# Performance work log

Hardware: AMD Instinct MI355X
Metric: run time of the kernel (lower is better)

The kernel has to match this reference:

```python
import jax, jax.numpy as jnp
from jax import lax
import numpy as np

S = 2        # scale_factor
K = 5        # upsample_kernel_size
M = 64       # m_channels
C_IN = 128

def setup_inputs() -> dict:
    key = jax.random.key(0)
    k1, k2, k3, k4, k5 = jax.random.split(key, 5)
    B, C, H, W = 8, C_IN, 64, 64
    x = jax.random.normal(k1, (B, C, H, W), dtype=jnp.float32)
    compress_w = jax.random.normal(k2, (M, C, 1, 1), dtype=jnp.float32) * 0.05
    compress_b = jax.random.normal(k3, (M,), dtype=jnp.float32) * 0.05
    n_out = K * K * S * S  # 100
    encoder_w = jax.random.normal(k4, (n_out, M, 3, 3), dtype=jnp.float32) * 0.05
    encoder_b = jax.random.normal(k5, (n_out,), dtype=jnp.float32) * 0.05
    return {"x": x, "compress_w": compress_w, "compress_b": compress_b,
            "encoder_w": encoder_w, "encoder_b": encoder_b}

def _carafe(x, compress_w, compress_b, encoder_w, encoder_b):
    B, C, H, W = x.shape
    k, s = K, S
    nH, nW = s * H, s * W
    # 1x1 compress conv
    m = jnp.einsum('bchw,mc->bmhw', x, compress_w[:, :, 0, 0]) + compress_b[None, :, None, None]
    # 3x3 encoder conv, stride 1, pad 1 (SAME)
    ker = lax.conv_general_dilated(m, encoder_w, window_strides=(1, 1), padding='SAME',
                                   dimension_numbers=('NCHW', 'OIHW', 'NCHW'))
    ker = ker + encoder_b[None, :, None, None]  # (B, k*k*s*s, H, W)
    # PixelShuffle(s): (B, k*k, s, s, H, W) -> (B, k*k, H, s, W, s) -> (B, k*k, nH, nW)
    ker = ker.reshape(B, k * k, s, s, H, W).transpose(0, 1, 4, 2, 5, 3).reshape(B, k * k, nH, nW)
    ker = jax.nn.softmax(ker, axis=1)
    # Unfold(k, stride=1, pad=k//2): stack k*k shifted views, ordering (kh outer, kw inner)
    pad = k // 2
    xp = jnp.pad(x, ((0, 0), (0, 0), (pad, pad), (pad, pad)))
    patches = jnp.stack([xp[:, :, i:i + H, j:j + W] for i in range(k) for j in range(k)],
                        axis=2)  # (B, C, k*k, H, W)
    # nearest upsample by s on spatial dims
    up = jnp.repeat(jnp.repeat(patches, s, axis=3), s, axis=4)  # (B, C, k*k, nH, nW)
    # weighted local sum
    out = jnp.sum(up * ker[:, None, :, :, :], axis=2)  # (B, C, nH, nW)
    return out

def reference(x, compress_w, compress_b, encoder_w, encoder_b):
    return _carafe(x, compress_w, compress_b, encoder_w, encoder_b)
```

## Files before the change

### kernel.cpp

```cpp
#include <hip/hip_runtime.h>
#include <math.h>


typedef __attribute__((ext_vector_type(8))) short short8;
typedef __attribute__((ext_vector_type(4))) float floatx4;
typedef __attribute__((ext_vector_type(2))) float v2f;

__device__ __forceinline__ unsigned short f2bf(float f) {
  union { float f; unsigned int u; } v; v.f = f;
  unsigned int u = v.u + 0x7fffu + ((v.u >> 16) & 1u);
  return (unsigned short)(u >> 16);
}
__device__ __forceinline__ void unpack2(unsigned int u, float& lo, float& hi) {
  union { unsigned int u; float f; } a, b;
  a.u = u << 16; b.u = u & 0xffff0000u;
  lo = a.f; hi = b.f;
}
__device__ __forceinline__ v2f unpack2v(unsigned int u) {
  union { unsigned int u; float f; } a, b;
  a.u = u << 16; b.u = u & 0xffff0000u;
  return (v2f){a.f, b.f};
}

__global__ __launch_bounds__(256) void k_prep_pad(
    const float* __restrict__ ew, const float* __restrict__ cw,
    unsigned short* __restrict__ a_prep, float* __restrict__ cwT,
    unsigned short* __restrict__ xpad) {
  const int blk = blockIdx.x;
  if (blk < 2448) {
    int idx = blk * 256 + (int)threadIdx.x;
    *(uint4*)&xpad[(size_t)idx * 8] = make_uint4(0u, 0u, 0u, 0u);
  } else {
    int idx = (blk - 2448) * 256 + (int)threadIdx.x;
    if (idx < 9 * 128 * 64) {
      int mo = idx & 63;
      int n = (idx >> 6) & 127;
      int tap = idx >> 13;
      float v = (n < 100) ? ew[(n * 64 + mo) * 9 + tap] : 0.f;
      a_prep[idx] = f2bf(v);
    } else {
      int r = idx - 9 * 128 * 64;
      int c = r >> 6, mo = r & 63;
      cwT[c * 64 + mo] = cw[mo * 128 + c];
    }
  }
}

__global__ __launch_bounds__(256) void k_compress(
    const float* __restrict__ x, const float* __restrict__ cwT,
    const float* __restrict__ cb, unsigned short* __restrict__ m_t,
    unsigned short* __restrict__ xpad) {
  __shared__ __align__(16) unsigned short ms[64][72];
  const int b = blockIdx.x >> 6;
  const int h = blockIdx.x & 63;
  const int wv = __builtin_amdgcn_readfirstlane((int)(threadIdx.x >> 6));
  const int lane = (int)(threadIdx.x & 63);
  const int mo0 = wv * 16;

  float acc[16];
#pragma unroll
  for (int k = 0; k < 16; ++k) acc[k] = 0.f;

  const float* xp = x + (((size_t)b * 128) * 64 + h) * 64 + lane;
  const float* wp = cwT + mo0;
  unsigned short* xpd =
      xpad + ((size_t)(b * 128) * 4896) + (h + 2) * 72 + 2 + lane;

#pragma unroll 4
  for (int c = 0; c < 128; ++c) {
    float xv = xp[(size_t)c * 4096];
    if ((c >> 5) == wv)
      xpd[(size_t)c * 4896] = f2bf(xv);
#pragma unroll
    for (int k = 0; k < 16; ++k)
      acc[k] = fmaf(xv, wp[c * 64 + k], acc[k]);
  }

#pragma unroll
  for (int k = 0; k < 16; ++k) acc[k] += cb[mo0 + k];

#pragma unroll
  for (int k = 0; k < 8; ++k) {
    unsigned int p = ((unsigned int)f2bf(acc[2 * k + 1]) << 16) | f2bf(acc[2 * k]);
    *(unsigned int*)&ms[lane][mo0 + 2 * k] = p;
  }
  __syncthreads();
  const int t = threadIdx.x;
#pragma unroll
  for (int rep = 0; rep < 2; ++rep) {
    int idx = t + rep * 256;
    uint4 v = *(const uint4*)&ms[idx >> 3][(idx & 7) * 8];
    *(uint4*)&m_t[(size_t)blockIdx.x * 4096 + idx * 8] = v;
  }
}

__global__ __launch_bounds__(512, 4) void k_main(
    const unsigned short* __restrict__ m_t, const unsigned short* __restrict__ a_prep,
    const float* __restrict__ eb, const unsigned short* __restrict__ xpad,
    float* __restrict__ out) {
  __shared__ __align__(16) float raw[128 * 66];
  unsigned short* m_s = (unsigned short*)raw;
  unsigned short* wgt_s = (unsigned short*)raw;
  const int b = blockIdx.x >> 6;
  const int h = blockIdx.x & 63;
  const int t = threadIdx.x;

  for (int idx = t; idx < 3 * 64 * 8; idx += 512) {
    int r = idx >> 9;
    int rem = idx & 511;
    int w = rem >> 3, u = rem & 7;
    int hh = h + r - 1;
    uint4 val = make_uint4(0u, 0u, 0u, 0u);
    if (hh >= 0 && hh < 64)
      val = *(const uint4*)&m_t[(((b * 64 + hh) * 64 + w) * 64) + u * 8];
    *(uint4*)&m_s[(r * 64 + w) * 72 + u * 8] = val;
  }
  __syncthreads();

  const int wave = t >> 6, lane = t & 63;
  const int quad = lane >> 4, col = lane & 15;
  const int nbase = wave * 16;

  const floatx4 z4 = {0.f, 0.f, 0.f, 0.f};
  floatx4 acc[4];
#pragma unroll
  for (int p = 0; p < 4; ++p) acc[p] = z4;

  const short8 z8 = {0, 0, 0, 0, 0, 0, 0, 0};

#pragma unroll
  for (int tap = 0; tap < 9; ++tap) {
    const int dh = tap / 3, dw = tap % 3;
#pragma unroll
    for (int half = 0; half < 2; ++half) {
      const int mo0 = half * 32;
      short8 a0 = *(const short8*)&a_prep[((tap * 128 + nbase + col) * 64) + mo0 + quad * 8];
#pragma unroll
      for (int p = 0; p < 4; ++p) {
        int wsrc = p * 16 + col + dw - 1;
        int wc = min(max(wsrc, 0), 63);
        short8 bf = *(const short8*)&m_s[(dh * 64 + wc) * 72 + mo0 + quad * 8];
        if (wsrc < 0 || wsrc > 63) bf = z8;
        acc[p] = __builtin_amdgcn_mfma_f32_16x16x32_bf16(a0, bf, acc[p], 0, 0, 0);
      }
    }
  }

  __syncthreads();
#pragma unroll
  for (int p = 0; p < 4; ++p)
#pragma unroll
    for (int r = 0; r < 4; ++r)
      raw[(nbase + quad * 4 + r) * 66 + p * 16 + col] = acc[p][r];
  __syncthreads();

  float v[25];
  float inv = 0.f;
  if (t < 256) {
    const int q = wave;
    float mx = -1e30f;
#pragma unroll
    for (int kk = 0; kk < 25; ++kk) {
      v[kk] = raw[(kk * 4 + q) * 66 + lane] + eb[kk * 4 + q];
      mx = fmaxf(mx, v[kk]);
    }
    float s = 0.f;
#pragma unroll
    for (int kk = 0; kk < 25; ++kk) {
      v[kk] = __expf(v[kk] - mx);
      s += v[kk];
    }
    inv = 1.f / s;
  }
  __syncthreads();
  if (t < 256) {
    const int q = wave;
    const int ohl = q >> 1;
    const int owp = 2 * lane + (q & 1);
#pragma unroll
    for (int kk = 0; kk < 25; ++kk)
      wgt_s[(ohl * 25 + kk) * 128 + owp] = f2bf(v[kk] * inv);
  }
  __syncthreads();

  const int wg = t & 15;
  const int cg = t >> 4;
  const int w0 = wg * 4;
  const int c0 = cg * 4;

  const unsigned short* xb =
      xpad + ((size_t)(b * 128 + c0) * 4896) + h * 72 + w0;

  v2f accB[2][4][4];
#pragma unroll
  for (int oh = 0; oh < 2; ++oh)
#pragma unroll
    for (int ch = 0; ch < 4; ++ch)
#pragma unroll
      for (int k = 0; k < 4; ++k) accB[oh][ch][k] = (v2f){0.f, 0.f};

  for (int i = 0; i < 5; ++i) {
    float xr[4][8];
#pragma unroll
    for (int ch = 0; ch < 4; ++ch) {
      uint4 rawv = *(const uint4*)(xb + ch * 4896 + i * 72);
      unpack2(rawv.x, xr[ch][0], xr[ch][1]);
      unpack2(rawv.y, xr[ch][2], xr[ch][3]);
      unpack2(rawv.z, xr[ch][4], xr[ch][5]);
      unpack2(rawv.w, xr[ch][6], xr[ch][7]);
    }
#pragma unroll
    for (int j = 0; j < 5; ++j) {
      const int ij = i * 5 + j;
#pragma unroll
      for (int oh = 0; oh < 2; ++oh) {
        uint4 wr = *(const uint4*)&wgt_s[(oh * 25 + ij) * 128 + w0 * 2];
        v2f wp[4];
        wp[0] = unpack2v(wr.x);
        wp[1] = unpack2v(wr.y);
        wp[2] = unpack2v(wr.z);
        wp[3] = unpack2v(wr.w);
#pragma unroll
        for (int k = 0; k < 4; ++k)
#pragma unroll
          for (int ch = 0; ch < 4; ++ch) {
            float xv = xr[ch][k + j];
            v2f xvv = {xv, xv};
            accB[oh][ch][k] += xvv * wp[k];
          }
      }
    }
  }

#pragma unroll
  for (int ch = 0; ch < 4; ++ch)
#pragma unroll
    for (int oh = 0; oh < 2; ++oh) {
      float* orow =
          out + ((size_t)(b * 128 + c0 + ch) * 128 + (2 * h + oh)) * 128 + w0 * 2;
      float4 f0 = make_float4(accB[oh][ch][0].x, accB[oh][ch][0].y,
                              accB[oh][ch][1].x, accB[oh][ch][1].y);
      float4 f1 = make_float4(accB[oh][ch][2].x, accB[oh][ch][2].y,
                              accB[oh][ch][3].x, accB[oh][ch][3].y);
      *(float4*)orow = f0;
      *(float4*)(orow + 4) = f1;
    }
}

extern "C" void kernel_launch(void* const* d_in, const int* in_sizes, int n_in,
                              void* d_out, int out_size, void* d_ws, size_t ws_size,
                              hipStream_t stream) {
  (void)in_sizes; (void)n_in; (void)out_size; (void)ws_size;
  const float* x  = (const float*)d_in[0];
  const float* cw = (const float*)d_in[1];
  const float* cb = (const float*)d_in[2];
  const float* ew = (const float*)d_in[3];
  const float* eb = (const float*)d_in[4];
  float* out = (float*)d_out;

  char* wsb = (char*)d_ws;
  unsigned short* m_t    = (unsigned short*)(wsb);
  unsigned short* a_prep = (unsigned short*)(wsb + 4194304);
  unsigned short* xpad   = (unsigned short*)(wsb + 4341760);
  float*          cwT    = (float*)(wsb + 14368768);

  k_prep_pad<<<dim3(2768), dim3(256), 0, stream>>>(ew, cw, a_prep, cwT, xpad);
  k_compress<<<dim3(512), dim3(256), 0, stream>>>(x, cwT, cb, m_t, xpad);
  k_main<<<dim3(512), dim3(512), 0, stream>>>(m_t, a_prep, eb, xpad, out);
}
```

Measured before the change: 153.5 us.

## Halve k_main block size with more work per wave and swizzle block-to-row mapping

k_main now runs 256 threads per block instead of 512. Each wave computes two 16-row MFMA output tiles, sharing the B fragment loads, and every thread handles both channel halves in a loop in the weighted-sum phase, so all threads also take part in the softmax. Block indices in both k_compress and k_main are swizzled so that consecutive blocks map to rows spread across the image, which changes L2 and XCD locality for the neighbouring-row reads. This trades thread-level parallelism and occupancy constraints for more per-thread work and register pressure, and the launch bound no longer requests four blocks per CU.

```diff
diff --git a/kernel.cpp b/kernel.cpp
--- a/kernel.cpp
+++ b/kernel.cpp
@@ -20,6 +20,12 @@
   union { unsigned int u; float f; } a, b;
   a.u = u << 16; b.u = u & 0xffff0000u;
   return (v2f){a.f, b.f};
+}
+__device__ __forceinline__ void swizzle_bh(int blk, int& b, int& h) {
+  int x = blk & 7;
+  int i = blk >> 3;
+  b = i >> 3;
+  h = x * 8 + (i & 7);
 }
 
 __global__ __launch_bounds__(256) void k_prep_pad(
@@ -51,8 +57,8 @@
     const float* __restrict__ cb, unsigned short* __restrict__ m_t,
     unsigned short* __restrict__ xpad) {
   __shared__ __align__(16) unsigned short ms[64][72];
-  const int b = blockIdx.x >> 6;
-  const int h = blockIdx.x & 63;
+  int b, h;
+  swizzle_bh(blockIdx.x, b, h);
   const int wv = __builtin_amdgcn_readfirstlane((int)(threadIdx.x >> 6));
   const int lane = (int)(threadIdx.x & 63);
   const int mo0 = wv * 16;
@@ -86,45 +92,48 @@
   }
   __syncthreads();
   const int t = threadIdx.x;
+  const size_t mbase = (size_t)(b * 64 + h) * 4096;
 #pragma unroll
   for (int rep = 0; rep < 2; ++rep) {
     int idx = t + rep * 256;
     uint4 v = *(const uint4*)&ms[idx >> 3][(idx & 7) * 8];
-    *(uint4*)&m_t[(size_t)blockIdx.x * 4096 + idx * 8] = v;
-  }
-}
-
-__global__ __launch_bounds__(512, 4) void k_main(
+    *(uint4*)&m_t[mbase + idx * 8] = v;
+  }
+}
+
+__global__ __launch_bounds__(256) void k_main(
     const unsigned short* __restrict__ m_t, const unsigned short* __restrict__ a_prep,
     const float* __restrict__ eb, const unsigned short* __restrict__ xpad,
     float* __restrict__ out) {
   __shared__ __align__(16) float raw[128 * 66];
   unsigned short* m_s = (unsigned short*)raw;
   unsigned short* wgt_s = (unsigned short*)raw;
-  const int b = blockIdx.x >> 6;
-  const int h = blockIdx.x & 63;
+  int b, h;
+  swizzle_bh(blockIdx.x, b, h);
   const int t = threadIdx.x;
 
-  for (int idx = t; idx < 3 * 64 * 8; idx += 512) {
+  for (int idx = t; idx < 3 * 64 * 8; idx += 256) {
     int r = idx >> 9;
     int rem = idx & 511;
     int w = rem >> 3, u = rem & 7;
     int hh = h + r - 1;
     uint4 val = make_uint4(0u, 0u, 0u, 0u);
     if (hh >= 0 && hh < 64)
-      val = *(const uint4*)&m_t[(((b * 64 + hh) * 64 + w) * 64) + u * 8];
+      val = *(const uint4*)&m_t[(((size_t)(b * 64 + hh) * 64 + w) * 64) + u * 8];
     *(uint4*)&m_s[(r * 64 + w) * 72 + u * 8] = val;
   }
   __syncthreads();
 
   const int wave = t >> 6, lane = t & 63;
   const int quad = lane >> 4, col = lane & 15;
-  const int nbase = wave * 16;
+  const int nbase = wave * 32;
 
   const floatx4 z4 = {0.f, 0.f, 0.f, 0.f};
-  floatx4 acc[4];
-#pragma unroll
-  for (int p = 0; p < 4; ++p) acc[p] = z4;
+  floatx4 acc[2][4];
+#pragma unroll
+  for (int i = 0; i < 2; ++i)
+#pragma unroll
+    for (int p = 0; p < 4; ++p) acc[i][p] = z4;
 
   const short8 z8 = {0, 0, 0, 0, 0, 0, 0, 0};
 
@@ -135,46 +144,47 @@
     for (int half = 0; half < 2; ++half) {
       const int mo0 = half * 32;
       short8 a0 = *(const short8*)&a_prep[((tap * 128 + nbase + col) * 64) + mo0 + quad * 8];
+      short8 a1 = *(const short8*)&a_prep[((tap * 128 + nbase + 16 + col) * 64) + mo0 + quad * 8];
 #pragma unroll
       for (int p = 0; p < 4; ++p) {
         int wsrc = p * 16 + col + dw - 1;
         int wc = min(max(wsrc, 0), 63);
         short8 bf = *(const short8*)&m_s[(dh * 64 + wc) * 72 + mo0 + quad * 8];
         if (wsrc < 0 || wsrc > 63) bf = z8;
-        acc[p] = __builtin_amdgcn_mfma_f32_16x16x32_bf16(a0, bf, acc[p], 0, 0, 0);
+        acc[0][p] = __builtin_amdgcn_mfma_f32_16x16x32_bf16(a0, bf, acc[0][p], 0, 0, 0);
+        acc[1][p] = __builtin_amdgcn_mfma_f32_16x16x32_bf16(a1, bf, acc[1][p], 0, 0, 0);
       }
     }
   }
 
   __syncthreads();
 #pragma unroll
-  for (int p = 0; p < 4; ++p)
-#pragma unroll
-    for (int r = 0; r < 4; ++r)
-      raw[(nbase + quad * 4 + r) * 66 + p * 16 + col] = acc[p][r];
-  __syncthreads();
-
+  for (int i = 0; i < 2; ++i)
+#pragma unroll
+    for (int p = 0; p < 4; ++p)
+#pragma unroll
+      for (int r = 0; r < 4; ++r)
+        raw[(nbase + i * 16 + quad * 4 + r) * 66 + p * 16 + col] = acc[i][p][r];
+  __syncthreads();
+
+  const int q = wave;
   float v[25];
-  float inv = 0.f;
-  if (t < 256) {
-    const int q = wave;
-    float mx = -1e30f;
-#pragma unroll
-    for (int kk = 0; kk < 25; ++kk) {
-      v[kk] = raw[(kk * 4 + q) * 66 + lane] + eb[kk * 4 + q];
-      mx = fmaxf(mx, v[kk]);
-    }
-    float s = 0.f;
-#pragma unroll
-    for (int kk = 0; kk < 25; ++kk) {
-      v[kk] = __expf(v[kk] - mx);
-      s += v[kk];
-    }
-    inv = 1.f / s;
-  }
-  __syncthreads();
-  if (t < 256) {
-    const int q = wave;
+  float mx = -1e30f;
+#pragma unroll
+  for (int kk = 0; kk < 25; ++kk) {
+    v[kk] = raw[(kk * 4 + q) * 66 + lane] + eb[kk * 4 + q];
+    mx = fmaxf(mx, v[kk]);
+  }
+  float s = 0.f;
+#pragma unroll
+  for (int kk = 0; kk < 25; ++kk) {
+    v[kk] = __expf(v[kk] - mx);
+    s += v[kk];
+  }
+  float inv = 1.f / s;
+
+  __syncthreads();
+  {
     const int ohl = q >> 1;
     const int owp = 2 * lane + (q & 1);
 #pragma unroll
@@ -186,65 +196,67 @@
   const int wg = t & 15;
   const int cg = t >> 4;
   const int w0 = wg * 4;
-  const int c0 = cg * 4;
-
-  const unsigned short* xb =
-      xpad + ((size_t)(b * 128 + c0) * 4896) + h * 72 + w0;
-
-  v2f accB[2][4][4];
-#pragma unroll
-  for (int oh = 0; oh < 2; ++oh)
+
+  for (int chalf = 0; chalf < 2; ++chalf) {
+    const int c0 = chalf * 64 + cg * 4;
+    const unsigned short* xb =
+        xpad + ((size_t)(b * 128 + c0) * 4896) + h * 72 + w0;
+
+    v2f accB[2][4][4];
+#pragma unroll
+    for (int oh = 0; oh < 2; ++oh)
+#pragma unroll
+      for (int ch = 0; ch < 4; ++ch)
+#pragma unroll
+        for (int k = 0; k < 4; ++k) accB[oh][ch][k] = (v2f){0.f, 0.f};
+
+    for (int i = 0; i < 5; ++i) {
+      float xr[4][8];
+#pragma unroll
+      for (int ch = 0; ch < 4; ++ch) {
+        uint4 rawv = *(const uint4*)(xb + ch * 4896 + i * 72);
+        unpack2(rawv.x, xr[ch][0], xr[ch][1]);
+        unpack2(rawv.y, xr[ch][2], xr[ch][3]);
+        unpack2(rawv.z, xr[ch][4], xr[ch][5]);
+        unpack2(rawv.w, xr[ch][6], xr[ch][7]);
+      }
+#pragma unroll
+      for (int j = 0; j < 5; ++j) {
+        const int ij = i * 5 + j;
+#pragma unroll
+        for (int oh = 0; oh < 2; ++oh) {
+          uint4 wr = *(const uint4*)&wgt_s[(oh * 25 + ij) * 128 + w0 * 2];
+          v2f wp[4];
+          wp[0] = unpack2v(wr.x);
+          wp[1] = unpack2v(wr.y);
+          wp[2] = unpack2v(wr.z);
+          wp[3] = unpack2v(wr.w);
+#pragma unroll
+          for (int k = 0; k < 4; ++k)
+#pragma unroll
+            for (int ch = 0; ch < 4; ++ch) {
+              float xv = xr[ch][k + j];
+              v2f xvv = {xv, xv};
+              accB[oh][ch][k] += xvv * wp[k];
+            }
+        }
+      }
+    }
+
 #pragma unroll
     for (int ch = 0; ch < 4; ++ch)
 #pragma unroll
-      for (int k = 0; k < 4; ++k) accB[oh][ch][k] = (v2f){0.f, 0.f};
-
-  for (int i = 0; i < 5; ++i) {
-    float xr[4][8];
-#pragma unroll
-    for (int ch = 0; ch < 4; ++ch) {
-      uint4 rawv = *(const uint4*)(xb + ch * 4896 + i * 72);
-      unpack2(rawv.x, xr[ch][0], xr[ch][1]);
-      unpack2(rawv.y, xr[ch][2], xr[ch][3]);
-      unpack2(rawv.z, xr[ch][4], xr[ch][5]);
-      unpack2(rawv.w, xr[ch][6], xr[ch][7]);
-    }
-#pragma unroll
-    for (int j = 0; j < 5; ++j) {
-      const int ij = i * 5 + j;
-#pragma unroll
       for (int oh = 0; oh < 2; ++oh) {
-        uint4 wr = *(const uint4*)&wgt_s[(oh * 25 + ij) * 128 + w0 * 2];
-        v2f wp[4];
-        wp[0] = unpack2v(wr.x);
-        wp[1] = unpack2v(wr.y);
-        wp[2] = unpack2v(wr.z);
-        wp[3] = unpack2v(wr.w);
-#pragma unroll
-        for (int k = 0; k < 4; ++k)
-#pragma unroll
-          for (int ch = 0; ch < 4; ++ch) {
-            float xv = xr[ch][k + j];
-            v2f xvv = {xv, xv};
-            accB[oh][ch][k] += xvv * wp[k];
-          }
-      }
-    }
-  }
-
-#pragma unroll
-  for (int ch = 0; ch < 4; ++ch)
-#pragma unroll
-    for (int oh = 0; oh < 2; ++oh) {
-      float* orow =
-          out + ((size_t)(b * 128 + c0 + ch) * 128 + (2 * h + oh)) * 128 + w0 * 2;
-      float4 f0 = make_float4(accB[oh][ch][0].x, accB[oh][ch][0].y,
-                              accB[oh][ch][1].x, accB[oh][ch][1].y);
-      float4 f1 = make_float4(accB[oh][ch][2].x, accB[oh][ch][2].y,
-                              accB[oh][ch][3].x, accB[oh][ch][3].y);
-      *(float4*)orow = f0;
-      *(float4*)(orow + 4) = f1;
-    }
+        float* orow =
+            out + ((size_t)(b * 128 + c0 + ch) * 128 + (2 * h + oh)) * 128 + w0 * 2;
+        float4 f0 = make_float4(accB[oh][ch][0].x, accB[oh][ch][0].y,
+                                accB[oh][ch][1].x, accB[oh][ch][1].y);
+        float4 f1 = make_float4(accB[oh][ch][2].x, accB[oh][ch][2].y,
+                                accB[oh][ch][3].x, accB[oh][ch][3].y);
+        *(float4*)orow = f0;
+        *(float4*)(orow + 4) = f1;
+      }
+  }
 }
 
 extern "C" void kernel_launch(void* const* d_in, const int* in_sizes, int n_in,
@@ -266,5 +278,5 @@
 
   k_prep_pad<<<dim3(2768), dim3(256), 0, stream>>>(ew, cw, a_prep, cwT, xpad);
   k_compress<<<dim3(512), dim3(256), 0, stream>>>(x, cwT, cb, m_t, xpad);
-  k_main<<<dim3(512), dim3(512), 0, stream>>>(m_t, a_prep, eb, xpad, out);
-}
+  k_main<<<dim3(512), dim3(256), 0, stream>>>(m_t, a_prep, eb, xpad, out);
+}
```

Result: faster. 145.7 us (-5.1%).
